# Optimization experiments

Measured on AMD Instinct MI355X. Metric: run time of the kernel, lower is better.

## Reference

```python
import jax, jax.numpy as jnp
import numpy as np

B, T, V, D, HD, NH, L, F, MD = 16, 512, 2048, 512, 64, 8, 6, 2048, 16


def setup_inputs() -> dict:
    key = jax.random.key(0)
    ks = jax.random.split(key, 12)
    s = 0.02
    def n(k, shape):
        return jax.random.normal(k, shape, jnp.float32) * s
    return {
        "idx": jax.random.randint(ks[0], (B, T), 0, V),
        "emb": n(ks[1], (V, D)),
        "Wq": n(ks[2], (L, D, HD)), "bq": jnp.zeros((L, HD), jnp.float32),
        "Wk": n(ks[3], (L, D, HD)), "bk": jnp.zeros((L, HD), jnp.float32),
        "Wv": n(ks[4], (L, D, HD)), "bv": jnp.zeros((L, HD), jnp.float32),
        "rel_table": n(ks[5], (L, 2 * MD + 1, HD)),
        "Wo": n(ks[6], (L, NH * HD, D)), "bo": jnp.zeros((L, D), jnp.float32),
        "g1": jnp.ones((L, D), jnp.float32), "be1": jnp.zeros((L, D), jnp.float32),
        "g2": jnp.ones((L, D), jnp.float32), "be2": jnp.zeros((L, D), jnp.float32),
        "W1": n(ks[7], (L, D, F)), "b1": jnp.zeros((L, F), jnp.float32),
        "W2": n(ks[8], (L, F, D)), "b2": jnp.zeros((L, D), jnp.float32),
        "Wout": n(ks[9], (D, V)), "bout": jnp.zeros((V,), jnp.float32),
    }


def _pos_encoding(t_len, d):
    # NOTE: replicates repo bug: exponent is 2*i/d with i already even.
    pos = jnp.arange(t_len, dtype=jnp.float32)[:, None]
    i = jnp.arange(0, d, 2, dtype=jnp.float32)[None, :]
    ang = pos / jnp.power(jnp.float32(10000.0), 2.0 * i / d)
    pe = jnp.zeros((t_len, d), jnp.float32)
    pe = pe.at[:, 0::2].set(jnp.sin(ang))
    pe = pe.at[:, 1::2].set(jnp.cos(ang))
    return pe


def _ln(x, g, b):
    m = jnp.mean(x, -1, keepdims=True)
    v = jnp.var(x, -1, keepdims=True)  # biased variance, as torch LayerNorm
    return (x - m) / jnp.sqrt(v + 1e-5) * g + b


def reference(idx, emb, Wq, bq, Wk, bk, Wv, bv, rel_table, Wo, bo,
              g1, be1, g2, be2, W1, b1, W2, b2, Wout, bout):
    t_len = idx.shape[1]
    x = emb[idx]                                   # [B,T,D]
    h = 2.0 * x + _pos_encoding(t_len, D)          # forward adds x + (x + pe)
    t = jnp.arange(t_len)
    dm = jnp.clip(t[None, :] - t[:, None], -MD, MD) + MD  # dm[a,b] = clamp(b-a)
    causal = t[:, None] >= t[None, :]
    scale = 1.0 / jnp.sqrt(jnp.float32(HD))
    neg_inf = jnp.float32(-jnp.inf)
    for l in range(L):
        y = _ln(h, g1[l], be1[l])
        Q = y @ Wq[l] + bq[l]                      # [B,T,HD]
        K = y @ Wk[l] + bk[l]
        Vv = y @ Wv[l] + bv[l]
        bias = rel_table[l][dm]                    # [T,T,HD]; k_bias == v_bias in source
        scores = jnp.einsum('bth,bsh->bts', Q, K)
        rel = jnp.einsum('bth,tsh->bts', Q, bias)
        att = jax.nn.softmax(jnp.where(causal, (scores + rel) * scale, neg_inf), axis=-1)
        vals = jnp.einsum('bts,bsh->bth', att, Vv) + jnp.einsum('bts,tsh->bth', att, bias)
        cat = jnp.tile(vals, (1, 1, NH))           # all NH heads share one module's weights
        h = h + cat @ Wo[l] + bo[l]
        y2 = _ln(h, g2[l], be2[l])
        h = h + jax.nn.relu(y2 @ W1[l] + b1[l]) @ W2[l] + b2[l]
    return h @ Wout + bout                         # [B,T,V]
```

## Files before the change

### kernel.cpp

```cpp
#include <hip/hip_runtime.h>
#include <hip/hip_bf16.h>
#include <math.h>

#define BB 16
#define TT 512
#define VV 2048
#define DD 512
#define HDD 64
#define LL 6
#define FF 2048
#define BT 8192

typedef __hip_bfloat16 bf16;
typedef __attribute__((ext_vector_type(8))) short bf8s;
typedef __attribute__((ext_vector_type(4))) float f4;

__device__ __forceinline__ float cvt(float x){ return x; }
__device__ __forceinline__ float cvt(bf16 x){ return __bfloat162float(x); }

__device__ __forceinline__ void gl16(const bf16* g, bf16* l){
  __builtin_amdgcn_global_load_lds(
      (const __attribute__((address_space(1))) void*)g,
      (__attribute__((address_space(3))) void*)l,
      16, 0, 0);
}

__global__ void k_flag(const void* g1, int* flagp){
  if(threadIdx.x==0 && blockIdx.x==0){
    const unsigned short* u = (const unsigned short*)g1;
    *flagp = (u[0] == 0) ? 1 : 0;
  }
}

__global__ __launch_bounds__(256) void k_cvt_all(
    const void* rel, const void* bo, const void* g1, const void* be1,
    const void* g2, const void* be2, const void* b1, const void* b2,
    const void* bout, const void* bq, const void* bk, const void* bv,
    bf16* d_rel, bf16* d_bo, bf16* d_g1, bf16* d_be1,
    bf16* d_g2, bf16* d_be2, bf16* d_b1, bf16* d_b2,
    bf16* d_bout, bf16* d_bqkv, const int* __restrict__ flagp){
  int i = blockIdx.x*256 + threadIdx.x;
  bool isf = *flagp;
  auto ld = [&](const void* s, int k)->float{
    return isf ? ((const float*)s)[k] : cvt(((const bf16*)s)[k]);
  };
  if(i < 12672){ d_rel[i] = (bf16)ld(rel, i); return; } i -= 12672;
  if(i < 3072){ d_bo[i]  = (bf16)ld(bo, i);  return; } i -= 3072;
  if(i < 3072){ d_g1[i]  = (bf16)ld(g1, i);  return; } i -= 3072;
  if(i < 3072){ d_be1[i] = (bf16)ld(be1, i); return; } i -= 3072;
  if(i < 3072){ d_g2[i]  = (bf16)ld(g2, i);  return; } i -= 3072;
  if(i < 3072){ d_be2[i] = (bf16)ld(be2, i); return; } i -= 3072;
  if(i < 12288){ d_b1[i] = (bf16)ld(b1, i);  return; } i -= 12288;
  if(i < 3072){ d_b2[i]  = (bf16)ld(b2, i);  return; } i -= 3072;
  if(i < 2048){ d_bout[i]= (bf16)ld(bout, i);return; } i -= 2048;
  if(i < 384){ int l=i>>6, hh=i&63; d_bqkv[l*192 + hh]       = (bf16)ld(bq, i); return; } i -= 384;
  if(i < 384){ int l=i>>6, hh=i&63; d_bqkv[l*192 + 64 + hh]  = (bf16)ld(bk, i); return; } i -= 384;
  if(i < 384){ int l=i>>6, hh=i&63; d_bqkv[l*192 + 128 + hh] = (bf16)ld(bv, i); return; }
}

__global__ __launch_bounds__(256) void k_tr(const void* __restrict__ src, bf16* __restrict__ dst,
                                            int R, int C, long long sS, long long sD, int ldD,
                                            const int* __restrict__ flagp){
  __shared__ bf16 t[32][33];
  int z = blockIdx.z;
  int c0 = blockIdx.x*32, r0 = blockIdx.y*32;
  int tx = threadIdx.x & 31, ty = threadIdx.x >> 5;
  bool isf = flagp && (*flagp);
  const float* sf = (const float*)src;
  const bf16*  sb = (const bf16*)src;
  for(int i=ty; i<32; i+=8){
    size_t off = (size_t)z*sS + (size_t)(r0+i)*C + (c0+tx);
    float v = isf ? sf[off] : cvt(sb[off]);
    t[i][tx] = (bf16)v;
  }
  __syncthreads();
  for(int i=ty; i<32; i+=8){
    dst[(size_t)z*sD + (size_t)(c0+i)*ldD + (r0+tx)] = t[tx][i];
  }
}

__global__ __launch_bounds__(256) void k_tr3(const void* __restrict__ Wq, const void* __restrict__ Wk,
                                             const void* __restrict__ Wv, bf16* __restrict__ dst,
                                             const int* __restrict__ flagp){
  __shared__ bf16 t[32][33];
  int z = blockIdx.z;
  int j = z % 3, lz = z / 3;
  const void* src = (j==0) ? Wq : ((j==1) ? Wk : Wv);
  int c0 = blockIdx.x*32, r0 = blockIdx.y*32;
  int tx = threadIdx.x & 31, ty = threadIdx.x >> 5;
  bool isf = (*flagp);
  const float* sf = (const float*)src;
  const bf16*  sb = (const bf16*)src;
  for(int i=ty; i<32; i+=8){
    size_t off = (size_t)lz*512*64 + (size_t)(r0+i)*64 + (c0+tx);
    float v = isf ? sf[off] : cvt(sb[off]);
    t[i][tx] = (bf16)v;
  }
  __syncthreads();
  for(int i=ty; i<32; i+=8){
    dst[(size_t)lz*3*64*512 + (size_t)j*64*512 + (size_t)(c0+i)*512 + (r0+tx)] = t[tx][i];
  }
}

__global__ __launch_bounds__(256) void k_wsumT(const void* __restrict__ Wo,
                                               bf16* __restrict__ wsT,
                                               const int* __restrict__ flagp){
  int i = blockIdx.x*256 + threadIdx.x;
  if(i >= LL*64*512) return;
  int l = i >> 15, j = i & 32767, hh = j>>9, d = j&511;
  size_t loff = (size_t)l*512*512;
  bool isf = *flagp;
  float a = 0.f;
  #pragma unroll
  for(int n=0;n<8;++n){
    size_t idx = loff + (size_t)(n*64+hh)*512 + d;
    a += isf ? ((const float*)Wo)[idx] : cvt(((const bf16*)Wo)[idx]);
  }
  wsT[(size_t)l*32768 + d*64 + hh] = (bf16)a;
}

__global__ __launch_bounds__(256) void k_embed(const int* __restrict__ idx,
                                               const void* __restrict__ emb,
                                               float* __restrict__ h,
                                               const int* __restrict__ flagp){
  int r = blockIdx.x;
  int t = r & (TT-1);
  int tok = idx[r];
  bool isf = *flagp;
  for(int d = threadIdx.x; d < DD; d += 256){
    int p = d >> 1;
    float ang = (float)t * powf(10000.f, -(float)p * (1.f/128.f));
    float pe = (d & 1) ? cosf(ang) : sinf(ang);
    size_t off = (size_t)tok*DD + d;
    float ev = isf ? ((const float*)emb)[off] : cvt(((const bf16*)emb)[off]);
    h[(size_t)r*DD + d] = 2.f*ev + pe;
  }
}

__global__ __launch_bounds__(256) void k_ln(const float* __restrict__ x,
                                            const bf16* __restrict__ g,
                                            const bf16* __restrict__ b,
                                            bf16* __restrict__ y){
  int r = blockIdx.x;
  int tid = threadIdx.x;
  const float* xr = x + (size_t)r*DD;
  float v0 = xr[tid], v1 = xr[tid+256];
  float s = v0+v1, s2 = v0*v0 + v1*v1;
  for(int o=32;o;o>>=1){ s += __shfl_down(s,o); s2 += __shfl_down(s2,o); }
  __shared__ float red[8];
  int wv = tid>>6, ln = tid&63;
  if(ln==0){ red[wv]=s; red[4+wv]=s2; }
  __syncthreads();
  float a  = red[0]+red[1]+red[2]+red[3];
  float a2 = red[4]+red[5]+red[6]+red[7];
  float m  = a*(1.f/DD);
  float var = a2*(1.f/DD) - m*m;
  float inv = rsqrtf(var + 1e-5f);
  y[(size_t)r*DD+tid]     = (bf16)((v0-m)*inv*cvt(g[tid])     + cvt(b[tid]));
  y[(size_t)r*DD+tid+256] = (bf16)((v1-m)*inv*cvt(g[tid+256]) + cvt(b[tid+256]));
}

template<int BM,int BN,int WM,int WN,int CMODE,bool RELU,bool RESID,bool TRV>
__global__ __launch_bounds__(WM*WN*64) void mm(const bf16* __restrict__ A,
                                          const bf16* __restrict__ Bt,
                                          void* __restrict__ Cv,
                                          const bf16* __restrict__ bias,
                                          int M, int N, int K,
                                          long long sA, long long sB, long long sC, int sBias,
                                          int gx,
                                          const int* __restrict__ flagp,
                                          bf16* __restrict__ vtr){
  constexpr int BK  = 64;
  constexpr int NT  = WM*WN*64;
  constexpr int FM  = BM/(WM*16);
  constexpr int FN  = BN/(WN*16);
  constexpr int S   = (BM+BN)*BK;
  constexpr int CAW = (BM*BK/512)/(NT/64);
  constexpr int CBW = (BN*BK/512)/(NT/64);
  __shared__ bf16 lds[2*S];
  int nwg = gridDim.x, bid = blockIdx.x;
  int q = nwg>>3, rr = nwg&7, xcd = bid&7, ii = bid>>3;
  int wg = (xcd<rr ? xcd*(q+1) : rr*(q+1)+(xcd-rr)*q) + ii;
  int bx = wg % gx, by = wg / gx;
  int z = blockIdx.z;
  A  += (size_t)z*sA;
  Bt += (size_t)z*sB;
  if(bias) bias += (size_t)z*sBias;
  int tid = threadIdx.x, lane = tid&63, w = tid>>6;
  int m0 = by*BM, n0 = bx*BN;
  int wrow = (w/WN)*(FM*16), wcol = (w%WN)*(FN*16);
  int l15 = lane&15, l4 = lane>>4;
  int lrow = lane>>3, lgr = lane&7;
  int nk = K/BK;
  auto stage = [&](int kt, int buf){
    bf16* Ab = lds + buf*S;
    bf16* Bb = Ab + BM*BK;
    const bf16* gA = A + (size_t)m0*K + kt*BK;
    const bf16* gB = Bt + (size_t)n0*K + kt*BK;
    #pragma unroll
    for(int i=0;i<CAW;++i){
      int chunk = w*CAW + i;
      int row = chunk*8 + lrow;
      gl16(gA + (size_t)row*K + ((lgr ^ (row&7))*8), Ab + chunk*512);
    }
    #pragma unroll
    for(int i=0;i<CBW;++i){
      int chunk = w*CBW + i;
      int row = chunk*8 + lrow;
      gl16(gB + (size_t)row*K + ((lgr ^ (row&7))*8), Bb + chunk*512);
    }
  };
  f4 acc[FM][FN] = {};
  stage(0, 0);
  __syncthreads();
  for(int kt=0; kt<nk; ++kt){
    int cur = kt & 1;
    if(kt+1 < nk) stage(kt+1, cur^1);
    const bf16* Ab = lds + cur*S;
    const bf16* Bb = Ab + BM*BK;
    #pragma unroll
    for(int g=0; g<2; ++g){
      bf8s af[FM], bfv[FN];
      #pragma unroll
      for(int i=0;i<FM;++i){
        int r = wrow + i*16 + l15;
        af[i] = *(const bf8s*)(Ab + r*BK + (((g*4+l4) ^ (r&7))*8));
      }
      #pragma unroll
      for(int j=0;j<FN;++j){
        int r = wcol + j*16 + l15;
        bfv[j] = *(const bf8s*)(Bb + r*BK + (((g*4+l4) ^ (r&7))*8));
      }
      #pragma unroll
      for(int i=0;i<FM;++i)
        #pragma unroll
        for(int j=0;j<FN;++j)
          acc[i][j] = __builtin_amdgcn_mfma_f32_16x16x32_bf16(af[i], bfv[j], acc[i][j], 0,0,0);
    }
    __syncthreads();
  }
  bool f32o = (CMODE==2) ? (*flagp != 0) : (CMODE==1);
  bool trv = TRV && (z == 2);
  #pragma unroll
  for(int i=0;i<FM;++i){
    #pragma unroll
    for(int j=0;j<FN;++j){
      int col = n0 + wcol + j*16 + l15;
      float bv = bias ? cvt(bias[col]) : 0.f;
      #pragma unroll
      for(int q2=0;q2<4;++q2){
        int row = m0 + wrow + i*16 + l4*4 + q2;
        float v = acc[i][j][q2] + bv;
        if(trv){
          int b = row >> 9, t = row & 511;
          vtr[(size_t)b*(64*512) + (size_t)col*512 + t] = (bf16)v;
          continue;
        }
        size_t off = (size_t)z*sC + (size_t)row*N + col;
        if(RESID) v += ((const float*)Cv)[off];
        if(RELU)  v = fmaxf(v, 0.f);
        if(CMODE==0)      ((bf16*)Cv)[off] = (bf16)v;
        else if(CMODE==1) ((float*)Cv)[off] = v;
        else if(CMODE==3) vtr[off] = (bf16)v;
        else { if(f32o) ((float*)Cv)[off] = v; else ((bf16*)Cv)[off] = (bf16)v; }
      }
    }
  }
}

__global__ __launch_bounds__(256) void k_attnproj(const bf16* __restrict__ Q,
                                                  const bf16* __restrict__ K,
                                                  const bf16* __restrict__ VbT,
                                                  const bf16* __restrict__ rel,
                                                  const bf16* __restrict__ wsT,
                                                  const bf16* __restrict__ bo,
                                                  const bf16* __restrict__ g,
                                                  const bf16* __restrict__ be,
                                                  float* __restrict__ h,
                                                  bf16* __restrict__ y){
  int ti = blockIdx.x, b = blockIdx.y;
  int t0 = ti*16;
  int tid = threadIdx.x, lane = tid & 63, wc = tid >> 6;
  int l15 = lane & 15, l4 = lane >> 4;
  __shared__ bf16  Plds[16][520];
  __shared__ bf16  vlds[16][68];
  __shared__ float qrs[16][17];
  __shared__ float amlds[16][17];
  __shared__ float redmx[4][16];
  __shared__ float redsum[4][16];
  __shared__ float rs[4][16], rs2[4][16];
  int nj = ti + 1;
  int KC = (nj*16 + 31) >> 5;

  const bf16* Qb = Q + ((size_t)b*512 + t0)*64;
  const bf16* Kb = K + (size_t)b*512*64;
  const bf16* Vb = VbT + (size_t)b*64*512;

  for(int i=tid; i<16*17; i+=256) ((float*)amlds)[i] = 0.f;
  if(nj & 1) Plds[tid>>4][nj*16 + (tid&15)] = (bf16)0.f;

  bf8s af0 = *(const bf8s*)(Qb + (size_t)l15*64 + l4*8);
  bf8s af1 = *(const bf8s*)(Qb + (size_t)l15*64 + 32 + l4*8);

  if(wc < 2){
    f4 qa = {};
    bf8s r0 = *(const bf8s*)(rel + (size_t)(wc*16+l15)*64 + l4*8);
    bf8s r1 = *(const bf8s*)(rel + (size_t)(wc*16+l15)*64 + 32 + l4*8);
    qa = __builtin_amdgcn_mfma_f32_16x16x32_bf16(af0, r0, qa, 0,0,0);
    qa = __builtin_amdgcn_mfma_f32_16x16x32_bf16(af1, r1, qa, 0,0,0);
    int m = wc*16 + l15;
    if(m < 17){
      #pragma unroll
      for(int q=0;q<4;++q) qrs[l4*4+q][m] = qa[q];
    }
  }
  __syncthreads();

  float mx4[4] = {-INFINITY,-INFINITY,-INFINITY,-INFINITY};
  for(int j=wc; j<nj; j+=4){
    f4 sa = {};
    const bf16* kr = Kb + (size_t)(j*16+l15)*64;
    bf8s k0 = *(const bf8s*)(kr + l4*8);
    bf8s k1 = *(const bf8s*)(kr + 32 + l4*8);
    sa = __builtin_amdgcn_mfma_f32_16x16x32_bf16(af0, k0, sa, 0,0,0);
    sa = __builtin_amdgcn_mfma_f32_16x16x32_bf16(af1, k1, sa, 0,0,0);
    int s = j*16 + l15;
    #pragma unroll
    for(int q=0;q<4;++q){
      int row = l4*4+q, t = t0+row;
      float sp = -1e30f;
      if(s <= t){
        int m = s - t + 16; m = m < 0 ? 0 : m;
        sp = (sa[q] + qrs[row][m])*0.125f;
        mx4[q] = fmaxf(mx4[q], sp);
      }
      Plds[row][s] = (bf16)sp;
    }
  }
  #pragma unroll
  for(int q=0;q<4;++q){
    float m = mx4[q];
    m = fmaxf(m, __shfl_xor(m,1)); m = fmaxf(m, __shfl_xor(m,2));
    m = fmaxf(m, __shfl_xor(m,4)); m = fmaxf(m, __shfl_xor(m,8));
    mx4[q] = m;
  }
  if(l15==0){
    #pragma unroll
    for(int q=0;q<4;++q) redmx[wc][l4*4+q] = mx4[q];
  }
  __syncthreads();

  float mxg[4], sum4[4] = {0.f,0.f,0.f,0.f};
  #pragma unroll
  for(int q=0;q<4;++q){
    int rloc = l4*4+q;
    mxg[q] = fmaxf(fmaxf(redmx[0][rloc], redmx[1][rloc]),
                   fmaxf(redmx[2][rloc], redmx[3][rloc]));
  }
  for(int j=wc; j<nj; j+=4){
    int s = j*16 + l15;
    #pragma unroll
    for(int q=0;q<4;++q){
      int row = l4*4+q, t = t0+row;
      float e = expf(cvt(Plds[row][s]) - mxg[q]);
      Plds[row][s] = (bf16)e;
      sum4[q] += e;
      int m = s - t + 16;
      if(m >= 1 && m <= 16) amlds[row][m] = e;
    }
  }
  #pragma unroll
  for(int q=0;q<4;++q){
    float s = sum4[q];
    s += __shfl_xor(s,1); s += __shfl_xor(s,2);
    s += __shfl_xor(s,4); s += __shfl_xor(s,8);
    sum4[q] = s;
  }
  if(l15==0){
    #pragma unroll
    for(int q=0;q<4;++q) redsum[wc][l4*4+q] = sum4[q];
  }
  __syncthreads();

  f4 pacc = {0,0,0,0};
  for(int ks=0; ks<KC; ++ks){
    bf8s ap = *(const bf8s*)(&Plds[l15][ks*32 + l4*8]);
    bf8s bv = *(const bf8s*)(Vb + (size_t)(wc*16+l15)*512 + ks*32 + l4*8);
    pacc = __builtin_amdgcn_mfma_f32_16x16x32_bf16(ap, bv, pacc, 0,0,0);
  }
  #pragma unroll
  for(int q=0;q<4;++q){
    int row = l4*4+q;
    float sum = redsum[0][row]+redsum[1][row]+redsum[2][row]+redsum[3][row];
    float rsv = 1.f/sum;
    float a[16];
    float amsum = 0.f;
    #pragma unroll
    for(int m=1;m<=16;++m){ a[m-1] = amlds[row][m]; amsum += a[m-1]; }
    float am0 = sum - amsum;
    int hh = wc*16 + l15;
    float acc = pacc[q] + am0*cvt(rel[hh]);
    #pragma unroll
    for(int m=1;m<=16;++m) acc += a[m-1]*cvt(rel[m*64 + hh]);
    vlds[row][hh] = (bf16)(acc*rsv);
  }
  __syncthreads();

  bf8s pa0 = *(const bf8s*)(&vlds[l15][l4*8]);
  bf8s pa1 = *(const bf8s*)(&vlds[l15][32 + l4*8]);
  f4 acc2[8] = {};
  #pragma unroll
  for(int j=0;j<8;++j){
    int nn = wc*8 + j;
    bf8s bv0 = *(const bf8s*)(wsT + (size_t)(nn*16+l15)*64 + l4*8);
    bf8s bv1 = *(const bf8s*)(wsT + (size_t)(nn*16+l15)*64 + 32 + l4*8);
    acc2[j] = __builtin_amdgcn_mfma_f32_16x16x32_bf16(pa0, bv0, acc2[j], 0,0,0);
    acc2[j] = __builtin_amdgcn_mfma_f32_16x16x32_bf16(pa1, bv1, acc2[j], 0,0,0);
  }
  float s4[4] = {0,0,0,0}, s24[4] = {0,0,0,0};
  #pragma unroll
  for(int j=0;j<8;++j){
    int col = (wc*8+j)*16 + l15;
    float bv = cvt(bo[col]);
    #pragma unroll
    for(int q=0;q<4;++q){
      int row = t0 + l4*4 + q;
      size_t off = ((size_t)b*512 + row)*512 + col;
      float v = acc2[j][q] + bv + h[off];
      acc2[j][q] = v;
      h[off] = v;
      s4[q] += v; s24[q] += v*v;
    }
  }
  #pragma unroll
  for(int q=0;q<4;++q){
    #pragma unroll
    for(int o=1;o<16;o<<=1){ s4[q] += __shfl_xor(s4[q],o); s24[q] += __shfl_xor(s24[q],o); }
    if(l15==0){ rs[wc][l4*4+q] = s4[q]; rs2[wc][l4*4+q] = s24[q]; }
  }
  __syncthreads();
  #pragma unroll
  for(int q=0;q<4;++q){
    int rloc = l4*4+q;
    float a  = rs[0][rloc]+rs[1][rloc]+rs[2][rloc]+rs[3][rloc];
    float a2 = rs2[0][rloc]+rs2[1][rloc]+rs2[2][rloc]+rs2[3][rloc];
    float mean = a*(1.f/512.f);
    float var  = a2*(1.f/512.f) - mean*mean;
    float inv  = rsqrtf(var + 1e-5f);
    int row = t0 + rloc;
    #pragma unroll
    for(int j=0;j<8;++j){
      int col = (wc*8+j)*16 + l15;
      y[((size_t)b*512 + row)*512 + col] =
          (bf16)((acc2[j][q]-mean)*inv*cvt(g[col]) + cvt(be[col]));
    }
  }
}

extern "C" void kernel_launch(void* const* d_in, const int* in_sizes, int n_in,
                              void* d_out, int out_size, void* d_ws, size_t ws_size,
                              hipStream_t stream){
  const int* idx = (const int*)d_in[0];

  char* p = (char*)d_ws;
  auto alloc = [&](size_t bytes)->char*{ char* r = p; p += (bytes + 255) & ~(size_t)255; return r; };

  int*  flag  = (int*)alloc(4);
  bf16* rel_b = (bf16*)alloc(12672*2);
  bf16* bo_b  = (bf16*)alloc(3072*2);
  bf16* g1_b  = (bf16*)alloc(3072*2);
  bf16* be1_b = (bf16*)alloc(3072*2);
  bf16* g2_b  = (bf16*)alloc(3072*2);
  bf16* be2_b = (bf16*)alloc(3072*2);
  bf16* b1_b  = (bf16*)alloc(12288*2);
  bf16* b2_b  = (bf16*)alloc(3072*2);
  bf16* bout_b= (bf16*)alloc(2048*2);
  bf16* bqkv  = (bf16*)alloc(LL*192*2);
  bf16* WqkvT = (bf16*)alloc((size_t)LL*3*64*512*2);
  bf16* W1T   = (bf16*)alloc((size_t)LL*2048*512*2);
  bf16* W2T   = (bf16*)alloc((size_t)LL*512*2048*2);
  bf16* WoutT = (bf16*)alloc((size_t)2048*512*2);
  bf16* wsT_all=(bf16*)alloc((size_t)LL*512*64*2);
  float* h    = (float*)alloc((size_t)BT*DD*4);
  bf16*  y    = (bf16*) alloc((size_t)BT*DD*2);
  bf16*  hb   = y;
  bf16*  QKV  = (bf16*) alloc((size_t)3*BT*64*2);
  bf16*  VbT  = (bf16*) alloc((size_t)BB*64*512*2);
  bf16*  mid  = (bf16*)d_out;
  bf16*  Qb = QKV, *Kb = QKV + (size_t)BT*64;

  k_flag<<<1,64,0,stream>>>(d_in[11], flag);
  k_cvt_all<<<(46592+255)/256,256,0,stream>>>(
      d_in[8], d_in[10], d_in[11], d_in[12], d_in[13], d_in[14],
      d_in[16], d_in[18], d_in[20], d_in[3], d_in[5], d_in[7],
      rel_b, bo_b, g1_b, be1_b, g2_b, be2_b, b1_b, b2_b, bout_b, bqkv, flag);
  k_tr3<<<dim3(2,16,3*LL),256,0,stream>>>(d_in[2], d_in[4], d_in[6], WqkvT, flag);
  k_tr<<<dim3(64,16,LL),256,0,stream>>>(d_in[15], W1T, 512, 2048, 512*2048, 2048*512, 512, flag);
  k_tr<<<dim3(16,64,LL),256,0,stream>>>(d_in[17], W2T, 2048, 512, 2048*512, 512*2048, 2048, flag);
  k_tr<<<dim3(64,16,1),256,0,stream>>>(d_in[19], WoutT, 512, 2048, 0, 0, 512, flag);
  k_wsumT<<<(LL*32768+255)/256,256,0,stream>>>(d_in[9], wsT_all, flag);

  k_embed<<<BT,256,0,stream>>>(idx, d_in[1], h, flag);

  for(int l=0; l<LL; ++l){
    k_ln<<<BT,256,0,stream>>>(h, g1_b+l*DD, be1_b+l*DD, y);
    mm<32,64,2,2,0,false,false,true><<<dim3(256,1,3),256,0,stream>>>(
        y, WqkvT + (size_t)l*3*64*512, QKV, bqkv + l*192,
        BT, 64, 512, 0, 64*512, (long long)BT*64, 64, 1, nullptr, VbT);
    k_attnproj<<<dim3(32,16),256,0,stream>>>(Qb, Kb, VbT, rel_b + l*33*64,
                                             wsT_all + (size_t)l*32768,
                                             bo_b + l*DD, g2_b + l*DD, be2_b + l*DD, h, y);
    mm<128,128,2,2,0,true,false,false><<<dim3(1024,1,1),256,0,stream>>>(
        y, W1T + (size_t)l*2048*512, mid, b1_b + l*FF, BT, 2048, 512, 0,0,0,0, 16, nullptr, nullptr);
    if(l < LL-1){
      mm<128,64,4,1,1,false,true,false><<<dim3(512,1,1),256,0,stream>>>(
          mid, W2T + (size_t)l*512*2048, h, b2_b + l*DD, BT, 512, 2048, 0,0,0,0, 8, nullptr, nullptr);
    } else {
      mm<128,64,4,1,3,false,true,false><<<dim3(512,1,1),256,0,stream>>>(
          mid, W2T + (size_t)l*512*2048, h, b2_b + l*DD, BT, 512, 2048, 0,0,0,0, 8, nullptr, hb);
    }
  }
  mm<128,128,2,2,2,false,false,false><<<dim3(1024,1,1),256,0,stream>>>(
      hb, WoutT, d_out, bout_b, BT, 2048, 512, 0,0,0,0, 16, flag, nullptr);
}
```

Measured before the change: 721.3 us.

## Fuse pre-attention LayerNorm into the QKV projection kernel

Replaces the separate LayerNorm kernel and QKV GEMM with one kernel. Each block normalizes 32 rows of h into a swizzled LDS tile, then runs MFMA against all 192 QKV weight columns and writes Q/K plus transposed V. This removes a launch and the bf16 y round trip through global memory per layer. The cost is that B operands are read straight from global without LDS staging, the grid is only 256 blocks, and 64 floats per thread raise register pressure.

```diff
diff --git a/kernel.cpp b/kernel.cpp
--- a/kernel.cpp
+++ b/kernel.cpp
@@ -18,7 +18,7 @@
 __device__ __forceinline__ float cvt(float x){ return x; }
 __device__ __forceinline__ float cvt(bf16 x){ return __bfloat162float(x); }
 
-__device__ __forceinline__ void gl16(const bf16* g, bf16* l){
+__device__ __forceinline__ void gl16(const void* g, void* l){
   __builtin_amdgcn_global_load_lds(
       (const __attribute__((address_space(1))) void*)g,
       (__attribute__((address_space(3))) void*)l,
@@ -135,29 +135,6 @@
     float ev = isf ? ((const float*)emb)[off] : cvt(((const bf16*)emb)[off]);
     h[(size_t)r*DD + d] = 2.f*ev + pe;
   }
-}
-
-__global__ __launch_bounds__(256) void k_ln(const float* __restrict__ x,
-                                            const bf16* __restrict__ g,
-                                            const bf16* __restrict__ b,
-                                            bf16* __restrict__ y){
-  int r = blockIdx.x;
-  int tid = threadIdx.x;
-  const float* xr = x + (size_t)r*DD;
-  float v0 = xr[tid], v1 = xr[tid+256];
-  float s = v0+v1, s2 = v0*v0 + v1*v1;
-  for(int o=32;o;o>>=1){ s += __shfl_down(s,o); s2 += __shfl_down(s2,o); }
-  __shared__ float red[8];
-  int wv = tid>>6, ln = tid&63;
-  if(ln==0){ red[wv]=s; red[4+wv]=s2; }
-  __syncthreads();
-  float a  = red[0]+red[1]+red[2]+red[3];
-  float a2 = red[4]+red[5]+red[6]+red[7];
-  float m  = a*(1.f/DD);
-  float var = a2*(1.f/DD) - m*m;
-  float inv = rsqrtf(var + 1e-5f);
-  y[(size_t)r*DD+tid]     = (bf16)((v0-m)*inv*cvt(g[tid])     + cvt(b[tid]));
-  y[(size_t)r*DD+tid+256] = (bf16)((v1-m)*inv*cvt(g[tid+256]) + cvt(b[tid+256]));
 }
 
 template<int BM,int BN,int WM,int WN,int CMODE,bool RELU,bool RESID,bool TRV>
@@ -268,6 +245,82 @@
   }
 }
 
+__global__ __launch_bounds__(256) void k_lnqkv(const float* __restrict__ h,
+                                               const bf16* __restrict__ g,
+                                               const bf16* __restrict__ be,
+                                               const bf16* __restrict__ Wt,
+                                               const bf16* __restrict__ bqkv,
+                                               bf16* __restrict__ QKV,
+                                               bf16* __restrict__ VbT){
+  __shared__ bf16 Al[32*512];
+  int m0 = blockIdx.x*32;
+  int tid = threadIdx.x, lane = tid&63, w = tid>>6;
+  int l15 = lane&15, l4 = lane>>4;
+  int row = tid>>3, s8 = tid&7;
+  const float* hr = h + (size_t)(m0+row)*512 + s8*64;
+  float hv[64];
+  float s=0.f, s2=0.f;
+  #pragma unroll
+  for(int i=0;i<64;++i){ float v = hr[i]; hv[i]=v; s+=v; s2+=v*v; }
+  s += __shfl_xor(s,1); s2 += __shfl_xor(s2,1);
+  s += __shfl_xor(s,2); s2 += __shfl_xor(s2,2);
+  s += __shfl_xor(s,4); s2 += __shfl_xor(s2,4);
+  float mean = s*(1.f/512.f);
+  float var  = s2*(1.f/512.f) - mean*mean;
+  float inv  = rsqrtf(var + 1e-5f);
+  #pragma unroll
+  for(int j=0;j<8;++j){
+    int gidx = s8*8 + j;
+    bf8s pack;
+    #pragma unroll
+    for(int e=0;e<8;++e){
+      int col = s8*64 + j*8 + e;
+      bf16 yb = (bf16)((hv[j*8+e]-mean)*inv*cvt(g[col]) + cvt(be[col]));
+      short sb; __builtin_memcpy(&sb, &yb, 2);
+      pack[e] = sb;
+    }
+    *(bf8s*)(&Al[row*512 + ((gidx ^ (row&7))*8)]) = pack;
+  }
+  __syncthreads();
+  f4 acc[2][3] = {};
+  for(int kc=0; kc<16; ++kc){
+    bf8s af[2];
+    #pragma unroll
+    for(int i=0;i<2;++i){
+      int r = i*16 + l15;
+      af[i] = *(const bf8s*)(&Al[r*512 + (((kc*4+l4) ^ (r&7))*8)]);
+    }
+    #pragma unroll
+    for(int j=0;j<3;++j){
+      int n = (w*3+j)*16 + l15;
+      bf8s bv = *(const bf8s*)(Wt + (size_t)n*512 + kc*32 + l4*8);
+      #pragma unroll
+      for(int i=0;i<2;++i)
+        acc[i][j] = __builtin_amdgcn_mfma_f32_16x16x32_bf16(af[i], bv, acc[i][j], 0,0,0);
+    }
+  }
+  #pragma unroll
+  for(int j=0;j<3;++j){
+    int n = (w*3+j)*16 + l15;
+    int plane = n >> 6, hh = n & 63;
+    float bias = cvt(bqkv[n]);
+    #pragma unroll
+    for(int i=0;i<2;++i){
+      #pragma unroll
+      for(int q=0;q<4;++q){
+        int rg = m0 + i*16 + l4*4 + q;
+        float v = acc[i][j][q] + bias;
+        if(plane == 2){
+          int b = rg >> 9, t = rg & 511;
+          VbT[(size_t)b*64*512 + (size_t)hh*512 + t] = (bf16)v;
+        } else {
+          QKV[(size_t)plane*BT*64 + (size_t)rg*64 + hh] = (bf16)v;
+        }
+      }
+    }
+  }
+}
+
 __global__ __launch_bounds__(256) void k_attnproj(const bf16* __restrict__ Q,
                                                   const bf16* __restrict__ K,
                                                   const bf16* __restrict__ VbT,
@@ -503,10 +556,8 @@
   k_embed<<<BT,256,0,stream>>>(idx, d_in[1], h, flag);
 
   for(int l=0; l<LL; ++l){
-    k_ln<<<BT,256,0,stream>>>(h, g1_b+l*DD, be1_b+l*DD, y);
-    mm<32,64,2,2,0,false,false,true><<<dim3(256,1,3),256,0,stream>>>(
-        y, WqkvT + (size_t)l*3*64*512, QKV, bqkv + l*192,
-        BT, 64, 512, 0, 64*512, (long long)BT*64, 64, 1, nullptr, VbT);
+    k_lnqkv<<<256,256,0,stream>>>(h, g1_b+l*DD, be1_b+l*DD,
+                                  WqkvT + (size_t)l*3*64*512, bqkv + l*192, QKV, VbT);
     k_attnproj<<<dim3(32,16),256,0,stream>>>(Qb, Kb, VbT, rel_b + l*33*64,
                                              wsT_all + (size_t)l*32768,
                                              bo_b + l*DD, g2_b + l*DD, be2_b + l*DD, h, y);
```

Result: no change. 714.7 us (-0.9%).
